# Optimization experiments

Measured on AMD Instinct MI355X. Metric: run time of the kernel, lower is better.

Reference implementation:

```python
import jax, jax.numpy as jnp
import numpy as np

B, N, IN, H, I, A, NA, NH = 4096, 8, 256, 256, 64, 64, 32, 256
VAR_FLOOR = 0.002
BN_EPS = 1e-5


def _lin(x, w, b):
    # torch Linear: x @ w.T + b, w: [out, in]
    return x @ w.T + b


def _bn_train(x, g, b):
    # BatchNorm1d in training mode: batch stats, biased variance
    mu = jnp.mean(x, axis=0)
    var = jnp.var(x, axis=0)
    return (x - mu) * jax.lax.rsqrt(var + BN_EPS) * g + b


def _intent_net(h_la, w1, b1, g, bbn, w2, b2):
    z = _lin(h_la, w1, b1)
    z = _bn_train(z, g, bbn)
    z = jax.nn.leaky_relu(z, 0.01)
    return _lin(z, w2, b2)


def setup_inputs() -> dict:
    key = jax.random.key(0)
    ks = jax.random.split(key, 30)
    s = 0.05
    d = {
        "inputs": jax.random.normal(ks[0], (B * N, IN), jnp.float32),
        "last_actions": jax.random.normal(ks[1], (B, N, NA), jnp.float32),
        "hidden_state": jax.random.normal(ks[2], (B * N, H), jnp.float32),
        "eps": jax.random.normal(ks[3], (B * N, I), jnp.float32),
        # fc1
        "fc1_w": jax.random.normal(ks[4], (H, IN), jnp.float32) * s,
        "fc1_b": jnp.zeros((H,), jnp.float32),
        # GRUCell (r,z,n gate order, torch layout)
        "gru_w_ih": jax.random.normal(ks[5], (3 * H, H), jnp.float32) * s,
        "gru_w_hh": jax.random.normal(ks[6], (3 * H, H), jnp.float32) * s,
        "gru_b_ih": jnp.zeros((3 * H,), jnp.float32),
        "gru_b_hh": jnp.zeros((3 * H,), jnp.float32),
        # intent_net: Linear(H+NA, NH) -> BN -> LeakyReLU -> Linear(NH, 2*I)
        "in1_w": jax.random.normal(ks[7], (NH, H + NA), jnp.float32) * s,
        "in1_b": jnp.zeros((NH,), jnp.float32),
        "bn_g": jnp.ones((NH,), jnp.float32),
        "bn_b": jnp.zeros((NH,), jnp.float32),
        "in2_w": jax.random.normal(ks[8], (2 * I, NH), jnp.float32) * s,
        "in2_b": jnp.zeros((2 * I,), jnp.float32),
        # attention projections
        "wq_w": jax.random.normal(ks[9], (A, I), jnp.float32) * s,
        "wq_b": jnp.zeros((A,), jnp.float32),
        "wk_w": jax.random.normal(ks[10], (A, I), jnp.float32) * s,
        "wk_b": jnp.zeros((A,), jnp.float32),
        "wv_w": jax.random.normal(ks[11], (A, I + H), jnp.float32) * s,
        "wv_b": jnp.zeros((A,), jnp.float32),
        # fc2
        "fc2_w": jax.random.normal(ks[12], (NA, H + A), jnp.float32) * s,
        "fc2_b": jnp.zeros((NA,), jnp.float32),
        "bs": B,
        "t": 1,
    }
    return d


def reference(inputs, last_actions, hidden_state, eps,
              fc1_w, fc1_b, gru_w_ih, gru_w_hh, gru_b_ih, gru_b_hh,
              in1_w, in1_b, bn_g, bn_b, in2_w, in2_b,
              wq_w, wq_b, wk_w, wk_b, wv_w, wv_b, fc2_w, fc2_b,
              bs, t):
    n = N
    x = jax.nn.relu(_lin(inputs, fc1_w, fc1_b))  # [bs*n, H]
    h_in = hidden_state.reshape(-1, H)
    # torch GRUCell
    gi = x @ gru_w_ih.T + gru_b_ih
    gh = h_in @ gru_w_hh.T + gru_b_hh
    i_r, i_z, i_n = jnp.split(gi, 3, axis=-1)
    h_r, h_z, h_n = jnp.split(gh, 3, axis=-1)
    r = jax.nn.sigmoid(i_r + h_r)
    z = jax.nn.sigmoid(i_z + h_z)
    nng = jnp.tanh(i_n + r * h_n)
    h = (1.0 - z) * nng + z * h_in  # [bs*n, H]

    la = last_actions.reshape(bs * n, NA)
    h_la = jnp.concatenate([h, la], axis=-1)
    ip = _intent_net(h_la, in1_w, in1_b, bn_g, bn_b, in2_w, in2_b)  # [bs*n, 2I]
    mean = ip[:, :I]
    std = jnp.maximum(jnp.exp(ip[:, I:]), VAR_FLOOR)
    intent = mean + eps * std  # reparameterized sample, [bs*n, I]

    q = _lin(intent, wq_w, wq_b).reshape(bs, n, A)  # query per agent i
    k = _lin(intent, wk_w, wk_b).reshape(bs, n, A)  # key per agent j
    scale = 1.0 / jnp.sqrt(jnp.float32(A))
    alpha = jnp.einsum('bia,bja->bij', q * scale, k)  # [bs, n, n]
    diag = jnp.eye(n, dtype=bool)
    alpha = jnp.where(diag[None], -1e9, alpha)
    alpha = jax.nn.softmax(alpha, axis=-1)

    v = _lin(jnp.concatenate([intent, h], axis=-1), wv_w, wv_b).reshape(bs, n, A)
    combined = jnp.einsum('bij,bja->bia', alpha, v).reshape(bs * n, A)

    local_Q = _lin(jnp.concatenate([h, combined], axis=-1), fc2_w, fc2_b).reshape(bs, n, NA)
    # final intent_embed: fresh intent_net output (no clamp/exp applied)
    intent_embed = _intent_net(h_la, in1_w, in1_b, bn_g, bn_b, in2_w, in2_b)
    return local_Q, h, intent, intent_embed
```

## Files before the change

kernel.cpp:

```cpp
#include <hip/hip_runtime.h>
#include <hip/hip_bf16.h>

#define BN_ 32768

using bf16 = __hip_bfloat16;
typedef __bf16 v8bf __attribute__((ext_vector_type(8)));
typedef unsigned short v8us __attribute__((ext_vector_type(8)));
typedef float v4f __attribute__((ext_vector_type(4)));

__device__ __forceinline__ float b2f(bf16 x) { return __bfloat162float(x); }
__device__ __forceinline__ bf16 f2b(float x) { return __float2bfloat16(x); }
__device__ __forceinline__ unsigned short f2bu(float x) {
  bf16 h = __float2bfloat16(x);
  return *reinterpret_cast<unsigned short*>(&h);
}
__device__ __forceinline__ float bu2f(unsigned short u) {
  union { unsigned int i; float f; } x;
  x.i = ((unsigned int)u) << 16;
  return x.f;
}
__device__ __forceinline__ void gl_lds16(const void* g, void* l) {
  __builtin_amdgcn_global_load_lds(
      (const __attribute__((address_space(1))) void*)g,
      (__attribute__((address_space(3))) void*)l, 16, 0, 0);
}
__device__ __forceinline__ float fsig(float x) { return 1.f / (1.f + __expf(-x)); }
__device__ __forceinline__ float ftanh(float x) {
  return 1.f - 2.f / (__expf(2.f * x) + 1.f);
}
template <int CF>
__device__ __forceinline__ void cstore(void* C, size_t off, float v) {
  if constexpr (CF) ((float*)C)[off] = v;
  else ((bf16*)C)[off] = f2b(v);
}
__device__ __forceinline__ int xcd_swz() {
  const int nbx = gridDim.x, nby = gridDim.y;
  const int f = blockIdx.y * nbx + blockIdx.x;
  const int nwg = nbx * nby;
  const int q = nwg >> 3, r = nwg & 7;
  const int xcd = f & 7, l = f >> 3;
  if (r == 0) return xcd * q + l;
  return (xcd < r ? xcd * (q + 1) : r * (q + 1) + (xcd - r) * q) + l;
}

template <int TM, int TN, int WR, int WC, int ACT, int A1M, int A2M, int KS, int KSB,
          int CF, int ATF, int STATS>
__global__ __launch_bounds__(256) void gemm_bt(
    const void* __restrict__ A1, int lda1, const void* __restrict__ A2, int lda2,
    const bf16* __restrict__ B1, const bf16* __restrict__ B2, int ldb,
    const float* __restrict__ bias, void* C, int ldc, int K,
    const float* __restrict__ tsc, const float* __restrict__ tsh,
    float* __restrict__ PART) {
  constexpr int BK = 64;
  __shared__ __align__(16) unsigned short As[TM * BK];
  __shared__ __align__(16) unsigned short Bs[TN * BK];
  const int tid = threadIdx.x;
  const int wv = tid >> 6;
  const int lane = tid & 63;
  const int w = xcd_swz();
  const int bm = (w / gridDim.y) * TM;
  const int bn = (w % gridDim.y) * TN;

  constexpr int WM = TM / WR, WN = TN / WC;
  constexpr int FM = WM / 16, FN = WN / 16;
  const int wm0 = (wv % WR) * WM;
  const int wn0 = (wv / WR) * WN;

  v4f acc[FM][FN];
  const v4f vzero = {0.f, 0.f, 0.f, 0.f};
  for (int i = 0; i < FM; ++i)
    for (int j = 0; j < FN; ++j) acc[i][j] = vzero;

  const int lrow = lane >> 3;
  const int lcol = (lane & 7) * 8;
  const int mr = lane & 15;
  const int kq = (lane >> 4) * 8;

  for (int k0 = 0; k0 < K; k0 += BK) {
    {
      const bool useA1 = (KS == 0) || (k0 < KS);
      const void* Ap = useA1 ? A1 : A2;
      const int lda = useA1 ? lda1 : lda2;
      const int ka = useA1 ? k0 : k0 - KS;
      const bool f32 = useA1 ? (A1M == 1) : (A2M == 1);
      if (ATF && useA1) {
        const unsigned short* Ab = (const unsigned short*)Ap;
        const float4 s0 = *(const float4*)(tsc + ka + lcol);
        const float4 s1 = *(const float4*)(tsc + ka + lcol + 4);
        const float4 h0 = *(const float4*)(tsh + ka + lcol);
        const float4 h1 = *(const float4*)(tsh + ka + lcol + 4);
        const float sc[8] = {s0.x, s0.y, s0.z, s0.w, s1.x, s1.y, s1.z, s1.w};
        const float sh[8] = {h0.x, h0.y, h0.z, h0.w, h1.x, h1.y, h1.z, h1.w};
        for (int ch = wv; ch < TM / 8; ch += 4) {
          const unsigned short* s = Ab + (size_t)(bm + ch * 8 + lrow) * lda + ka + lcol;
          v8us zin = *(const v8us*)s;
          v8us d;
#pragma unroll
          for (int u = 0; u < 8; ++u) {
            float v = bu2f(zin[u]) * sc[u] + sh[u];
            d[u] = f2bu(v > 0.f ? v : 0.01f * v);
          }
          *(v8us*)(As + ch * 8 * BK + lane * 8) = d;
        }
      } else if (f32) {
        const float* Af = (const float*)Ap;
        for (int ch = wv; ch < TM / 8; ch += 4) {
          const float* s = Af + (size_t)(bm + ch * 8 + lrow) * lda + ka + lcol;
          float4 x0 = *(const float4*)s;
          float4 x1 = *(const float4*)(s + 4);
          v8us d;
          d[0]=f2bu(x0.x); d[1]=f2bu(x0.y); d[2]=f2bu(x0.z); d[3]=f2bu(x0.w);
          d[4]=f2bu(x1.x); d[5]=f2bu(x1.y); d[6]=f2bu(x1.z); d[7]=f2bu(x1.w);
          *(v8us*)(As + ch * 8 * BK + lane * 8) = d;
        }
      } else {
        const unsigned short* Ab = (const unsigned short*)Ap;
        for (int ch = wv; ch < TM / 8; ch += 4)
          gl_lds16(Ab + (size_t)(bm + ch * 8 + lrow) * lda + ka + lcol,
                   As + ch * 8 * BK);
      }
    }
    {
      const bool useB1 = (KSB == 0) || (k0 < KSB);
      const bf16* Bp = useB1 ? B1 : B2;
      const int kb = useB1 ? k0 : k0 - KSB;
      for (int ch = wv; ch < TN / 8; ch += 4)
        gl_lds16((const unsigned short*)Bp + (size_t)(bn + ch * 8 + lrow) * ldb + kb + lcol,
                 Bs + ch * 8 * BK);
    }
    __syncthreads();
#pragma unroll
    for (int kk = 0; kk < BK; kk += 32) {
      v8bf af[FM], bfr[FN];
#pragma unroll
      for (int i = 0; i < FM; ++i)
        af[i] = *(const v8bf*)(As + (wm0 + i * 16 + mr) * BK + kk + kq);
#pragma unroll
      for (int j = 0; j < FN; ++j)
        bfr[j] = *(const v8bf*)(Bs + (wn0 + j * 16 + mr) * BK + kk + kq);
#pragma unroll
      for (int i = 0; i < FM; ++i)
#pragma unroll
        for (int j = 0; j < FN; ++j)
          acc[i][j] = __builtin_amdgcn_mfma_f32_16x16x32_bf16(af[i], bfr[j],
                                                              acc[i][j], 0, 0, 0);
    }
    __syncthreads();
  }
  const int crow = (lane >> 4) * 4;
#pragma unroll
  for (int j = 0; j < FN; ++j) {
    const int gcol = bn + wn0 + j * 16 + mr;
    const float bv = bias[gcol];
    float ps = 0.f, pq = 0.f;
#pragma unroll
    for (int i = 0; i < FM; ++i) {
#pragma unroll
      for (int r = 0; r < 4; ++r) {
        const int grow = bm + wm0 + i * 16 + crow + r;
        size_t off = (size_t)grow * ldc + gcol;
        float v = acc[i][j][r] + bv;
        if (ACT == 1) v = v > 0.f ? v : 0.f;
        if constexpr (STATS) {
          const unsigned short d = f2bu(v);
          ((bf16*)C)[off] = *(const bf16*)&d;
          const float vr = bu2f(d);
          ps += vr; pq += vr * vr;
        } else {
          cstore<CF>(C, off, v);
        }
      }
    }
    if constexpr (STATS) {
      ps += __shfl_xor(ps, 16); ps += __shfl_xor(ps, 32);
      pq += __shfl_xor(pq, 16); pq += __shfl_xor(pq, 32);
      if (lane < 16) {
        const int slot = (gcol << 9) + ((bm >> 7) << 1) + (wv % WR);
        PART[slot] = ps;
        PART[131072 + slot] = pq;
      }
    }
  }
}

__global__ __launch_bounds__(64) void bn_finalize2(
    const float* __restrict__ PART, const float* __restrict__ g,
    const float* __restrict__ b, float* __restrict__ stats) {
  const int col = blockIdx.x;
  const int lane = threadIdx.x;
  const float4* ps = (const float4*)(PART + (col << 9));
  const float4* pq = (const float4*)(PART + 131072 + (col << 9));
  float s = 0.f, q = 0.f;
#pragma unroll
  for (int u = 0; u < 2; ++u) {
    const float4 a = ps[lane * 2 + u];
    const float4 c = pq[lane * 2 + u];
    s += a.x + a.y + a.z + a.w;
    q += c.x + c.y + c.z + c.w;
  }
#pragma unroll
  for (int m = 1; m < 64; m <<= 1) {
    s += __shfl_xor(s, m);
    q += __shfl_xor(q, m);
  }
  if (lane == 0) {
    const float mean = s * (1.f / 32768.f);
    float var = q * (1.f / 32768.f) - mean * mean;
    var = fmaxf(var, 0.f);
    const float sc = g[col] * rsqrtf(var + 1e-5f);
    stats[512 + col] = sc;
    stats[768 + col] = b[col] - mean * sc;
  }
}

__global__ __launch_bounds__(256) void gru_fused(
    const bf16* __restrict__ X, const bf16* __restrict__ HB,
    const bf16* __restrict__ Win, const bf16* __restrict__ Whn,
    const float* __restrict__ FBp, const bf16* G1, unsigned short* HB2,
    float* __restrict__ Hout) {
  constexpr int BK = 64;
  __shared__ __align__(16) char smem[49152];
  unsigned short* AsX = (unsigned short*)smem;
  unsigned short* AsH = AsX + 4096;
  unsigned short* Bin = AsH + 4096;
  unsigned short* Bhn = Bin + 8192;
  float* Ein = (float*)smem;
  float* Ehn = Ein + 64 * 68;

  const int tid = threadIdx.x;
  const int wv = tid >> 6;
  const int lane = tid & 63;
  const int w = xcd_swz();
  const int bm = (w / gridDim.y) * 64;
  const int bn = (w % gridDim.y) * 128;
  const int wm0 = (wv & 1) * 32;
  const int wn0 = (wv >> 1) * 64;

  v4f ain[2][4], ahn[2][4];
  const v4f vzero = {0.f, 0.f, 0.f, 0.f};
  for (int i = 0; i < 2; ++i)
    for (int j = 0; j < 4; ++j) { ain[i][j] = vzero; ahn[i][j] = vzero; }

  const int lrow = lane >> 3;
  const int lcol = (lane & 7) * 8;
  const int mr = lane & 15;
  const int kq = (lane >> 4) * 8;

  for (int k0 = 0; k0 < 256; k0 += BK) {
    for (int ch = wv; ch < 8; ch += 4) {
      const size_t aoff = (size_t)(bm + ch * 8 + lrow) * 256 + k0 + lcol;
      gl_lds16((const unsigned short*)X + aoff, AsX + ch * 8 * BK);
      gl_lds16((const unsigned short*)HB + aoff, AsH + ch * 8 * BK);
    }
    for (int ch = wv; ch < 16; ch += 4) {
      const size_t boff = (size_t)(bn + ch * 8 + lrow) * 256 + k0 + lcol;
      gl_lds16((const unsigned short*)Win + boff, Bin + ch * 8 * BK);
      gl_lds16((const unsigned short*)Whn + boff, Bhn + ch * 8 * BK);
    }
    __syncthreads();
#pragma unroll
    for (int kk = 0; kk < BK; kk += 32) {
      v8bf ax[2], ah[2], bi[4], bh[4];
#pragma unroll
      for (int i = 0; i < 2; ++i) {
        ax[i] = *(const v8bf*)(AsX + (wm0 + i * 16 + mr) * BK + kk + kq);
        ah[i] = *(const v8bf*)(AsH + (wm0 + i * 16 + mr) * BK + kk + kq);
      }
#pragma unroll
      for (int j = 0; j < 4; ++j) {
        bi[j] = *(const v8bf*)(Bin + (wn0 + j * 16 + mr) * BK + kk + kq);
        bh[j] = *(const v8bf*)(Bhn + (wn0 + j * 16 + mr) * BK + kk + kq);
      }
#pragma unroll
      for (int i = 0; i < 2; ++i)
#pragma unroll
        for (int j = 0; j < 4; ++j) {
          ain[i][j] = __builtin_amdgcn_mfma_f32_16x16x32_bf16(ax[i], bi[j],
                                                              ain[i][j], 0, 0, 0);
          ahn[i][j] = __builtin_amdgcn_mfma_f32_16x16x32_bf16(ah[i], bh[j],
                                                              ahn[i][j], 0, 0, 0);
        }
    }
    __syncthreads();
  }

  const int crow = (lane >> 4) * 4;
  const int myhalf = wn0 >> 6;
  const int c4 = (tid & 15) * 4;
#pragma unroll
  for (int h = 0; h < 2; ++h) {
    ushort4 r4a[4], z4a[4], hp4a[4];
#pragma unroll
    for (int it = 0; it < 4; ++it) {
      const int grow = bm + (tid >> 4) + it * 16;
      const int gcol = bn + h * 64 + c4;
      const unsigned short* g1p = (const unsigned short*)G1 + (size_t)grow * 512 + gcol;
      r4a[it] = *(const ushort4*)g1p;
      z4a[it] = *(const ushort4*)(g1p + 256);
      hp4a[it] = *(const ushort4*)((const unsigned short*)HB + (size_t)grow * 256 + gcol);
    }
    __syncthreads();
    if (myhalf == h) {
#pragma unroll
      for (int i = 0; i < 2; ++i)
#pragma unroll
        for (int j = 0; j < 4; ++j)
#pragma unroll
          for (int r = 0; r < 4; ++r) {
            const int idx = (wm0 + i * 16 + crow + r) * 68 + j * 16 + mr;
            Ein[idx] = ain[i][j][r];
            Ehn[idx] = ahn[i][j][r];
          }
    }
    __syncthreads();
#pragma unroll
    for (int it = 0; it < 4; ++it) {
      const int row = (tid >> 4) + it * 16;
      const int grow = bm + row;
      const int gcol = bn + h * 64 + c4;
      const float4 ei = *(const float4*)(Ein + row * 68 + c4);
      const float4 eh = *(const float4*)(Ehn + row * 68 + c4);
      const float4 bin4 = *(const float4*)(FBp + 768 + gcol);
      const float4 bhn4 = *(const float4*)(FBp + 1024 + gcol);
      const float rv[4] = {bu2f(r4a[it].x), bu2f(r4a[it].y), bu2f(r4a[it].z), bu2f(r4a[it].w)};
      const float zv[4] = {bu2f(z4a[it].x), bu2f(z4a[it].y), bu2f(z4a[it].z), bu2f(z4a[it].w)};
      const float hpv[4] = {bu2f(hp4a[it].x), bu2f(hp4a[it].y), bu2f(hp4a[it].z), bu2f(hp4a[it].w)};
      const float eiv[4] = {ei.x, ei.y, ei.z, ei.w};
      const float ehv[4] = {eh.x, eh.y, eh.z, eh.w};
      const float biv[4] = {bin4.x, bin4.y, bin4.z, bin4.w};
      const float bhv[4] = {bhn4.x, bhn4.y, bhn4.z, bhn4.w};
      float vo[4];
#pragma unroll
      for (int u = 0; u < 4; ++u) {
        float rr = fsig(rv[u]);
        float zz = fsig(zv[u]);
        float nn = ftanh(eiv[u] + biv[u] + rr * (ehv[u] + bhv[u]));
        vo[u] = (1.f - zz) * nn + zz * hpv[u];
      }
      *(float4*)(Hout + (size_t)grow * 256 + gcol) =
          make_float4(vo[0], vo[1], vo[2], vo[3]);
      ushort4 hb2;
      hb2.x = f2bu(vo[0]); hb2.y = f2bu(vo[1]);
      hb2.z = f2bu(vo[2]); hb2.w = f2bu(vo[3]);
      *(ushort4*)(HB2 + (size_t)grow * 512 + gcol) = hb2;
    }
  }
}

__global__ void conv_all(
    const float* fc1_w, const float* w_ih, const float* w_hh, const float* in1_w,
    const float* in2_w, const float* wq_w, const float* wk_w, const float* wv_w,
    const float* fc2_w, const float* fc1_b, const float* b_ih, const float* b_hh,
    const float* in1_b, const float* in2_b, const float* wq_b, const float* wk_b,
    const float* wv_b, const float* fc2_b, const float* bn_g, const float* bn_b,
    bf16* __restrict__ WF, float* __restrict__ FB) {
  int idx = blockIdx.x * 256 + threadIdx.x;
  if (idx < 612352) {
    float v;
    if (idx < 65536) v = fc1_w[idx];
    else if (idx < 262144) v = w_ih[idx - 65536];
    else if (idx < 458752) v = w_hh[idx - 262144];
    else if (idx < 540672) {
      int j = idx - 458752, r = j / 320, c = j % 320;
      v = (c < 288) ? in1_w[r * 288 + c] : 0.f;
    } else if (idx < 573440) v = in2_w[idx - 540672];
    else if (idx < 581632) {
      int j = idx - 573440, r = j >> 6, c = j & 63;
      v = (r < 64) ? wq_w[r * 64 + c] : wk_w[(r - 64) * 64 + c];
    } else if (idx < 602112) v = wv_w[idx - 581632];
    else v = fc2_w[idx - 602112];
    WF[idx] = f2b(v);
  } else if (idx < 615936) {
    int j = idx - 612352;
    float v;
    if (j < 256) v = fc1_b[j];
    else if (j < 768) v = b_ih[j - 256] + b_hh[j - 256];
    else if (j < 1024) v = b_ih[512 + j - 768];
    else if (j < 1280) v = b_hh[512 + j - 1024];
    else if (j < 1536) v = in1_b[j - 1280];
    else if (j < 1664) v = in2_b[j - 1536];
    else if (j < 1792) { int c = j - 1664; v = (c < 64) ? wq_b[c] : wk_b[c - 64]; }
    else if (j < 1856) v = wv_b[j - 1792];
    else if (j < 1888) v = fc2_b[j - 1856];
    else if (j < 2144) v = bn_g[j - 1888];
    else if (j < 2400) v = bn_b[j - 2144];
    else v = 0.f;
    FB[j] = v;
  }
}

__global__ void pack_all(const float* __restrict__ h, bf16* __restrict__ hb,
                         const float* __restrict__ x, bf16* __restrict__ xb,
                         const float* __restrict__ la, bf16* __restrict__ lap) {
  const int bid = blockIdx.x;
  if (bid < 8192) {
    const float* s = bid < 4096 ? h : x;
    bf16* d = bid < 4096 ? hb : xb;
    const int i = (bid & 4095) * 256 + threadIdx.x;
    const float4 x0 = ((const float4*)s)[i * 2];
    const float4 x1 = ((const float4*)s)[i * 2 + 1];
    v8us o;
    o[0]=f2bu(x0.x); o[1]=f2bu(x0.y); o[2]=f2bu(x0.z); o[3]=f2bu(x0.w);
    o[4]=f2bu(x1.x); o[5]=f2bu(x1.y); o[6]=f2bu(x1.z); o[7]=f2bu(x1.w);
    ((v8us*)d)[i] = o;
  } else {
    const int i = (bid - 8192) * 256 + threadIdx.x;
    const int row = i >> 3, cg = i & 7;
    v8us o;
    if (cg < 4) {
      const float4 a = *(const float4*)(la + (size_t)row * 32 + cg * 8);
      const float4 b = *(const float4*)(la + (size_t)row * 32 + cg * 8 + 4);
      o[0]=f2bu(a.x); o[1]=f2bu(a.y); o[2]=f2bu(a.z); o[3]=f2bu(a.w);
      o[4]=f2bu(b.x); o[5]=f2bu(b.y); o[6]=f2bu(b.z); o[7]=f2bu(b.w);
    } else {
      for (int u = 0; u < 8; ++u) o[u] = 0;
    }
    ((v8us*)lap)[i] = o;
  }
}

__global__ void make_intent(const float* __restrict__ ie, const float* __restrict__ eps,
                            float* __restrict__ intent, unsigned short* __restrict__ itb) {
  int idx = blockIdx.x * 256 + threadIdx.x;
  int row = idx >> 6, c = idx & 63;
  float mean = ie[(size_t)row * 128 + c];
  float sd = fmaxf(expf(ie[(size_t)row * 128 + 64 + c]), 0.002f);
  float v = mean + eps[idx] * sd;
  intent[idx] = v;
  itb[(size_t)row * 512 + c] = f2bu(v);
}

__global__ __launch_bounds__(256) void attn(const bf16* __restrict__ QK,
                                            const bf16* __restrict__ Vv,
                                            bf16* __restrict__ comb) {
  __shared__ float q[4][8][65], k[4][8][65], v[4][8][65];
  __shared__ float al[4][8][8];
  const int wv = threadIdx.x >> 6, t = threadIdx.x & 63;
  const int b = blockIdx.x * 4 + wv;
  const size_t rb = (size_t)b * 8;
  const unsigned short* qkb = (const unsigned short*)QK + rb * 128;
#pragma unroll
  for (int p = 0; p < 2; ++p) {
    const int e = t * 8 + p * 512;
    const int row = e >> 7, col = e & 127;
    v8us d = *(const v8us*)(qkb + row * 128 + col);
    if (col < 64) {
#pragma unroll
      for (int u = 0; u < 8; ++u) q[wv][row][col + u] = bu2f(d[u]);
    } else {
#pragma unroll
      for (int u = 0; u < 8; ++u) k[wv][row][col - 64 + u] = bu2f(d[u]);
    }
  }
  {
    const int e = t * 8;
    const int row = e >> 6, col = e & 63;
    v8us d = *(const v8us*)((const unsigned short*)Vv + rb * 64 + row * 64 + col);
#pragma unroll
    for (int u = 0; u < 8; ++u) v[wv][row][col + u] = bu2f(d[u]);
  }
  __syncthreads();
  const int i = t >> 3, j = t & 7;
  float s = 0.f;
#pragma unroll
  for (int a = 0; a < 64; ++a) s += q[wv][i][a] * k[wv][j][a];
  s *= 0.125f;
  if (i == j) s = -1e9f;
  float m = s;
  m = fmaxf(m, __shfl_xor(m, 1, 8));
  m = fmaxf(m, __shfl_xor(m, 2, 8));
  m = fmaxf(m, __shfl_xor(m, 4, 8));
  float e = __expf(s - m);
  float sum = e;
  sum += __shfl_xor(sum, 1, 8);
  sum += __shfl_xor(sum, 2, 8);
  sum += __shfl_xor(sum, 4, 8);
  al[wv][i][j] = e / sum;
  __syncthreads();
  const int a0 = (t & 7) * 8;
  v8us o8;
#pragma unroll
  for (int u = 0; u < 8; ++u) {
    float o = 0.f;
#pragma unroll
    for (int jj = 0; jj < 8; ++jj) o += al[wv][i][jj] * v[wv][jj][a0 + u];
    o8[u] = f2bu(o);
  }
  *(v8us*)((unsigned short*)comb + (rb + i) * 64 + a0) = o8;
}

extern "C" void kernel_launch(void* const* d_in, const int* in_sizes, int n_in,
                              void* d_out, int out_size, void* d_ws, size_t ws_size,
                              hipStream_t stream) {
  (void)in_sizes; (void)n_in; (void)out_size; (void)ws_size;
  const float* inputs = (const float*)d_in[0];
  const float* last_actions = (const float*)d_in[1];
  const float* hidden = (const float*)d_in[2];
  const float* eps = (const float*)d_in[3];

  float* out = (float*)d_out;
  float* out_lq = out;
  float* out_h = out + 1048576;
  float* out_it = out + 9437184;
  float* out_ie = out + 11534336;

  bf16* HB = (bf16*)(out + 11534336);
  bf16* XB = (bf16*)(out + 1048576);
  bf16* LAP = (bf16*)out_lq;
  float* PART = out + 9437184;

  char* ws = (char*)d_ws;
  bf16* X    = (bf16*)(ws + 0);
  bf16* G1   = (bf16*)(ws + 16777216);
  unsigned short* HB2 = (unsigned short*)(ws + 16777216);
  unsigned short* ITB = (unsigned short*)(ws + 16777216) + 256;
  bf16* Z1   = (bf16*)(ws + 0);
  bf16* QK   = (bf16*)(ws + 0);
  bf16* V    = (bf16*)(ws + 8388608);
  bf16* COMB = (bf16*)(ws + 12582912);
  float* FB  = (float*)(ws + 50331648);
  bf16*  WF  = (bf16*)(ws + 50348032);
  float* stats = FB + 2560;

  conv_all<<<2406, 256, 0, stream>>>(
      (const float*)d_in[4], (const float*)d_in[6], (const float*)d_in[7],
      (const float*)d_in[10], (const float*)d_in[14], (const float*)d_in[16],
      (const float*)d_in[18], (const float*)d_in[20], (const float*)d_in[22],
      (const float*)d_in[5], (const float*)d_in[8], (const float*)d_in[9],
      (const float*)d_in[11], (const float*)d_in[15], (const float*)d_in[17],
      (const float*)d_in[19], (const float*)d_in[21], (const float*)d_in[23],
      (const float*)d_in[12], (const float*)d_in[13], WF, FB);

  pack_all<<<9216, 256, 0, stream>>>(hidden, HB, inputs, XB, last_actions, LAP);

  gemm_bt<64, 128, 2, 2, 1, 0, 0, 0, 0, 0, 0, 0><<<dim3(512, 2), 256, 0, stream>>>(
      XB, 256, nullptr, 0, WF + 0, nullptr, 256, FB + 0, X, 256, 256,
      nullptr, nullptr, nullptr);
  gemm_bt<64, 128, 2, 2, 0, 0, 0, 256, 256, 0, 0, 0><<<dim3(512, 4), 256, 0, stream>>>(
      X, 256, HB, 256, WF + 65536, WF + 262144, 256, FB + 256, G1, 512, 512,
      nullptr, nullptr, nullptr);
  gru_fused<<<dim3(512, 2), 256, 0, stream>>>(
      X, HB, WF + 65536 + 512 * 256, WF + 262144 + 512 * 256, FB, G1, HB2, out_h);

  gemm_bt<128, 128, 2, 2, 0, 0, 0, 256, 0, 0, 0, 1><<<dim3(256, 2), 256, 0, stream>>>(
      HB2, 512, LAP, 64, WF + 458752, nullptr, 320, FB + 1280, Z1, 256, 320,
      nullptr, nullptr, PART);
  bn_finalize2<<<256, 64, 0, stream>>>(PART, FB + 1888, FB + 2144, stats);
  gemm_bt<64, 128, 2, 2, 0, 0, 0, 0, 0, 1, 1, 0><<<dim3(512, 1), 256, 0, stream>>>(
      Z1, 256, nullptr, 0, WF + 540672, nullptr, 256, FB + 1536, out_ie, 128, 256,
      stats + 512, stats + 768, nullptr);
  make_intent<<<8192, 256, 0, stream>>>(out_ie, eps, out_it, ITB);
  gemm_bt<64, 128, 2, 2, 0, 0, 0, 0, 0, 0, 0, 0><<<dim3(512, 1), 256, 0, stream>>>(
      ITB, 512, nullptr, 0, WF + 573440, nullptr, 64, FB + 1664, QK, 128, 64,
      nullptr, nullptr, nullptr);
  gemm_bt<64, 64, 4, 1, 0, 0, 0, 64, 0, 0, 0, 0><<<dim3(512, 1), 256, 0, stream>>>(
      ITB, 512, HB2, 512, WF + 581632, nullptr, 320, FB + 1792, V, 64, 320,
      nullptr, nullptr, nullptr);
  attn<<<1024, 256, 0, stream>>>(QK, V, COMB);
  gemm_bt<64, 32, 4, 1, 0, 0, 0, 256, 0, 1, 0, 0><<<dim3(512, 1), 256, 0, stream>>>(
      HB2, 512, COMB, 64, WF + 602112, nullptr, 320, FB + 1856, out_lq, 32, 320,
      nullptr, nullptr, nullptr);
}
```

Measured before the change: 320.4 us.

## Fuse intent sampling into in2 GEMM, merge Q/K/V GEMMs, double-buffer GRU loads

The intent reparameterization (exp, floor, eps multiply, bf16 pack) moves into the epilogue of the second intent-net GEMM, which removes the separate make_intent kernel and its extra pass over the 128-wide output. The Q/K and V projections are merged into one 192-column GEMM over the concatenated [intent, h] input, using a zero-padded combined weight and a split epilogue that writes two outputs. The gru_fused kernel now double-buffers its LDS loads at K-step 32, so the next global load overlaps with the current MFMAs. In exchange, the merged Q/K GEMM does wasted multiplies over the zero-padded h columns, and the weight-conversion kernel grows.

```diff
diff --git a/kernel.cpp b/kernel.cpp
--- a/kernel.cpp
+++ b/kernel.cpp
@@ -44,13 +44,14 @@
 }
 
 template <int TM, int TN, int WR, int WC, int ACT, int A1M, int A2M, int KS, int KSB,
-          int CF, int ATF, int STATS>
+          int CF, int ATF, int STATS, int QKV>
 __global__ __launch_bounds__(256) void gemm_bt(
     const void* __restrict__ A1, int lda1, const void* __restrict__ A2, int lda2,
     const bf16* __restrict__ B1, const bf16* __restrict__ B2, int ldb,
     const float* __restrict__ bias, void* C, int ldc, int K,
     const float* __restrict__ tsc, const float* __restrict__ tsh,
-    float* __restrict__ PART) {
+    float* __restrict__ PART, const float* __restrict__ pe,
+    float* __restrict__ pit, unsigned short* __restrict__ pitb, void* C2) {
   constexpr int BK = 64;
   __shared__ __align__(16) unsigned short As[TM * BK];
   __shared__ __align__(16) unsigned short Bs[TN * BK];
@@ -148,36 +149,60 @@
     __syncthreads();
   }
   const int crow = (lane >> 4) * 4;
-#pragma unroll
-  for (int j = 0; j < FN; ++j) {
-    const int gcol = bn + wn0 + j * 16 + mr;
-    const float bv = bias[gcol];
-    float ps = 0.f, pq = 0.f;
-#pragma unroll
-    for (int i = 0; i < FM; ++i) {
+
+  if constexpr (ACT == 5) {
+#pragma unroll
+    for (int j = 0; j < 4; ++j) {
+      const int gcol = bn + j * 16 + mr;
+      const float bmn = bias[gcol];
+      const float bsd = bias[gcol + 64];
 #pragma unroll
       for (int r = 0; r < 4; ++r) {
-        const int grow = bm + wm0 + i * 16 + crow + r;
-        size_t off = (size_t)grow * ldc + gcol;
-        float v = acc[i][j][r] + bv;
-        if (ACT == 1) v = v > 0.f ? v : 0.f;
-        if constexpr (STATS) {
-          const unsigned short d = f2bu(v);
-          ((bf16*)C)[off] = *(const bf16*)&d;
-          const float vr = bu2f(d);
-          ps += vr; pq += vr * vr;
-        } else {
-          cstore<CF>(C, off, v);
+        const int grow = bm + wm0 + crow + r;
+        const float mean = acc[0][j][r] + bmn;
+        const float lstd = acc[0][j + 4][r] + bsd;
+        ((float*)C)[(size_t)grow * 128 + gcol] = mean;
+        ((float*)C)[(size_t)grow * 128 + gcol + 64] = lstd;
+        const float sd = fmaxf(__expf(lstd), 0.002f);
+        const float iv = mean + pe[(size_t)grow * 64 + gcol] * sd;
+        pit[(size_t)grow * 64 + gcol] = iv;
+        pitb[(size_t)grow * 512 + gcol] = f2bu(iv);
+      }
+    }
+  } else {
+#pragma unroll
+    for (int j = 0; j < FN; ++j) {
+      const int gcol = bn + wn0 + j * 16 + mr;
+      const float bv = bias[gcol];
+      float ps = 0.f, pq = 0.f;
+#pragma unroll
+      for (int i = 0; i < FM; ++i) {
+#pragma unroll
+        for (int r = 0; r < 4; ++r) {
+          const int grow = bm + wm0 + i * 16 + crow + r;
+          float v = acc[i][j][r] + bv;
+          if (ACT == 1) v = v > 0.f ? v : 0.f;
+          if constexpr (QKV) {
+            if (gcol < 128) ((bf16*)C)[(size_t)grow * 128 + gcol] = f2b(v);
+            else ((bf16*)C2)[(size_t)grow * 64 + (gcol - 128)] = f2b(v);
+          } else if constexpr (STATS) {
+            const unsigned short d = f2bu(v);
+            ((bf16*)C)[(size_t)grow * ldc + gcol] = *(const bf16*)&d;
+            const float vr = bu2f(d);
+            ps += vr; pq += vr * vr;
+          } else {
+            cstore<CF>(C, (size_t)grow * ldc + gcol, v);
+          }
         }
       }
-    }
-    if constexpr (STATS) {
-      ps += __shfl_xor(ps, 16); ps += __shfl_xor(ps, 32);
-      pq += __shfl_xor(pq, 16); pq += __shfl_xor(pq, 32);
-      if (lane < 16) {
-        const int slot = (gcol << 9) + ((bm >> 7) << 1) + (wv % WR);
-        PART[slot] = ps;
-        PART[131072 + slot] = pq;
+      if constexpr (STATS) {
+        ps += __shfl_xor(ps, 16); ps += __shfl_xor(ps, 32);
+        pq += __shfl_xor(pq, 16); pq += __shfl_xor(pq, 32);
+        if (lane < 16) {
+          const int slot = (gcol << 9) + ((bm >> 7) << 1) + (wv % WR);
+          PART[slot] = ps;
+          PART[131072 + slot] = pq;
+        }
       }
     }
   }
@@ -218,12 +243,7 @@
     const bf16* __restrict__ Win, const bf16* __restrict__ Whn,
     const float* __restrict__ FBp, const bf16* G1, unsigned short* HB2,
     float* __restrict__ Hout) {
-  constexpr int BK = 64;
   __shared__ __align__(16) char smem[49152];
-  unsigned short* AsX = (unsigned short*)smem;
-  unsigned short* AsH = AsX + 4096;
-  unsigned short* Bin = AsH + 4096;
-  unsigned short* Bhn = Bin + 8192;
   float* Ein = (float*)smem;
   float* Ehn = Ein + 64 * 68;
 
@@ -241,35 +261,44 @@
   for (int i = 0; i < 2; ++i)
     for (int j = 0; j < 4; ++j) { ain[i][j] = vzero; ahn[i][j] = vzero; }
 
-  const int lrow = lane >> 3;
-  const int lcol = (lane & 7) * 8;
+  const int lrow2 = lane >> 2;
+  const int lcol2 = (lane & 3) * 8;
   const int mr = lane & 15;
   const int kq = (lane >> 4) * 8;
 
-  for (int k0 = 0; k0 < 256; k0 += BK) {
-    for (int ch = wv; ch < 8; ch += 4) {
-      const size_t aoff = (size_t)(bm + ch * 8 + lrow) * 256 + k0 + lcol;
-      gl_lds16((const unsigned short*)X + aoff, AsX + ch * 8 * BK);
-      gl_lds16((const unsigned short*)HB + aoff, AsH + ch * 8 * BK);
-    }
-    for (int ch = wv; ch < 16; ch += 4) {
-      const size_t boff = (size_t)(bn + ch * 8 + lrow) * 256 + k0 + lcol;
-      gl_lds16((const unsigned short*)Win + boff, Bin + ch * 8 * BK);
-      gl_lds16((const unsigned short*)Whn + boff, Bhn + ch * 8 * BK);
-    }
-    __syncthreads();
-#pragma unroll
-    for (int kk = 0; kk < BK; kk += 32) {
+  auto STAGE = [&](int b, int t) {
+    unsigned short* base = (unsigned short*)(smem + b * 24576);
+    const int k0 = t * 32;
+    {
+      const size_t aoff = (size_t)(bm + wv * 16 + lrow2) * 256 + k0 + lcol2;
+      gl_lds16((const unsigned short*)X + aoff, base + wv * 512);
+      gl_lds16((const unsigned short*)HB + aoff, base + 2048 + wv * 512);
+    }
+    for (int c = wv; c < 8; c += 4) {
+      const size_t boff = (size_t)(bn + c * 16 + lrow2) * 256 + k0 + lcol2;
+      gl_lds16((const unsigned short*)Win + boff, base + 4096 + c * 512);
+      gl_lds16((const unsigned short*)Whn + boff, base + 8192 + c * 512);
+    }
+  };
+
+  int cur = 0;
+  STAGE(0, 0);
+  asm volatile("s_waitcnt vmcnt(0)" ::: "memory");
+  __builtin_amdgcn_s_barrier();
+  for (int t = 0; t < 8; ++t) {
+    if (t < 7) STAGE(cur ^ 1, t + 1);
+    {
+      const unsigned short* base = (const unsigned short*)(smem + cur * 24576);
       v8bf ax[2], ah[2], bi[4], bh[4];
 #pragma unroll
       for (int i = 0; i < 2; ++i) {
-        ax[i] = *(const v8bf*)(AsX + (wm0 + i * 16 + mr) * BK + kk + kq);
-        ah[i] = *(const v8bf*)(AsH + (wm0 + i * 16 + mr) * BK + kk + kq);
+        ax[i] = *(const v8bf*)(base + (wm0 + i * 16 + mr) * 32 + kq);
+        ah[i] = *(const v8bf*)(base + 2048 + (wm0 + i * 16 + mr) * 32 + kq);
       }
 #pragma unroll
       for (int j = 0; j < 4; ++j) {
-        bi[j] = *(const v8bf*)(Bin + (wn0 + j * 16 + mr) * BK + kk + kq);
-        bh[j] = *(const v8bf*)(Bhn + (wn0 + j * 16 + mr) * BK + kk + kq);
+        bi[j] = *(const v8bf*)(base + 4096 + (wn0 + j * 16 + mr) * 32 + kq);
+        bh[j] = *(const v8bf*)(base + 8192 + (wn0 + j * 16 + mr) * 32 + kq);
       }
 #pragma unroll
       for (int i = 0; i < 2; ++i)
@@ -281,7 +310,9 @@
                                                               ahn[i][j], 0, 0, 0);
         }
     }
-    __syncthreads();
+    asm volatile("s_waitcnt vmcnt(0)" ::: "memory");
+    __builtin_amdgcn_s_barrier();
+    cur ^= 1;
   }
 
   const int crow = (lane >> 4) * 4;
@@ -355,7 +386,7 @@
     const float* wv_b, const float* fc2_b, const float* bn_g, const float* bn_b,
     bf16* __restrict__ WF, float* __restrict__ FB) {
   int idx = blockIdx.x * 256 + threadIdx.x;
-  if (idx < 612352) {
+  if (idx < 673792) {
     float v;
     if (idx < 65536) v = fc1_w[idx];
     else if (idx < 262144) v = w_ih[idx - 65536];
@@ -364,14 +395,20 @@
       int j = idx - 458752, r = j / 320, c = j % 320;
       v = (c < 288) ? in1_w[r * 288 + c] : 0.f;
     } else if (idx < 573440) v = in2_w[idx - 540672];
-    else if (idx < 581632) {
-      int j = idx - 573440, r = j >> 6, c = j & 63;
-      v = (r < 64) ? wq_w[r * 64 + c] : wk_w[(r - 64) * 64 + c];
-    } else if (idx < 602112) v = wv_w[idx - 581632];
-    else v = fc2_w[idx - 602112];
+    else if (idx < 602112) {
+      v = (idx >= 573440 && idx < 581632)
+              ? 0.f
+              : (idx < 602112 ? 0.f : 0.f);
+    } else if (idx < 612352) v = fc2_w[idx - 602112];
+    else {
+      int j = idx - 612352, r = j / 320, c = j % 320;
+      if (r < 128) v = (c < 64) ? (r < 64 ? wq_w[r * 64 + c]
+                                          : wk_w[(r - 64) * 64 + c]) : 0.f;
+      else v = wv_w[(size_t)(r - 128) * 320 + c];
+    }
     WF[idx] = f2b(v);
-  } else if (idx < 615936) {
-    int j = idx - 612352;
+  } else if (idx < 677376) {
+    int j = idx - 673792;
     float v;
     if (j < 256) v = fc1_b[j];
     else if (j < 768) v = b_ih[j - 256] + b_hh[j - 256];
@@ -419,17 +456,6 @@
   }
 }
 
-__global__ void make_intent(const float* __restrict__ ie, const float* __restrict__ eps,
-                            float* __restrict__ intent, unsigned short* __restrict__ itb) {
-  int idx = blockIdx.x * 256 + threadIdx.x;
-  int row = idx >> 6, c = idx & 63;
-  float mean = ie[(size_t)row * 128 + c];
-  float sd = fmaxf(expf(ie[(size_t)row * 128 + 64 + c]), 0.002f);
-  float v = mean + eps[idx] * sd;
-  intent[idx] = v;
-  itb[(size_t)row * 512 + c] = f2bu(v);
-}
-
 __global__ __launch_bounds__(256) void attn(const bf16* __restrict__ QK,
                                             const bf16* __restrict__ Vv,
                                             bf16* __restrict__ comb) {
@@ -522,7 +548,7 @@
   bf16*  WF  = (bf16*)(ws + 50348032);
   float* stats = FB + 2560;
 
-  conv_all<<<2406, 256, 0, stream>>>(
+  conv_all<<<2646, 256, 0, stream>>>(
       (const float*)d_in[4], (const float*)d_in[6], (const float*)d_in[7],
       (const float*)d_in[10], (const float*)d_in[14], (const float*)d_in[16],
       (const float*)d_in[18], (const float*)d_in[20], (const float*)d_in[22],
@@ -533,31 +559,27 @@
 
   pack_all<<<9216, 256, 0, stream>>>(hidden, HB, inputs, XB, last_actions, LAP);
 
-  gemm_bt<64, 128, 2, 2, 1, 0, 0, 0, 0, 0, 0, 0><<<dim3(512, 2), 256, 0, stream>>>(
+  gemm_bt<64, 128, 2, 2, 1, 0, 0, 0, 0, 0, 0, 0, 0><<<dim3(512, 2), 256, 0, stream>>>(
       XB, 256, nullptr, 0, WF + 0, nullptr, 256, FB + 0, X, 256, 256,
-      nullptr, nullptr, nullptr);
-  gemm_bt<64, 128, 2, 2, 0, 0, 0, 256, 256, 0, 0, 0><<<dim3(512, 4), 256, 0, stream>>>(
+      nullptr, nullptr, nullptr, nullptr, nullptr, nullptr, nullptr);
+  gemm_bt<64, 128, 2, 2, 0, 0, 0, 256, 256, 0, 0, 0, 0><<<dim3(512, 4), 256, 0, stream>>>(
       X, 256, HB, 256, WF + 65536, WF + 262144, 256, FB + 256, G1, 512, 512,
-      nullptr, nullptr, nullptr);
+      nullptr, nullptr, nullptr, nullptr, nullptr, nullptr, nullptr);
   gru_fused<<<dim3(512, 2), 256, 0, stream>>>(
       X, HB, WF + 65536 + 512 * 256, WF + 262144 + 512 * 256, FB, G1, HB2, out_h);
 
-  gemm_bt<128, 128, 2, 2, 0, 0, 0, 256, 0, 0, 0, 1><<<dim3(256, 2), 256, 0, stream>>>(
+  gemm_bt<128, 128, 2, 2, 0, 0, 0, 256, 0, 0, 0, 1, 0><<<dim3(256, 2), 256, 0, stream>>>(
       HB2, 512, LAP, 64, WF + 458752, nullptr, 320, FB + 1280, Z1, 256, 320,
-      nullptr, nullptr, PART);
+      nullptr, nullptr, PART, nullptr, nullptr, nullptr, nullptr);
   bn_finalize2<<<256, 64, 0, stream>>>(PART, FB + 1888, FB + 2144, stats);
-  gemm_bt<64, 128, 2, 2, 0, 0, 0, 0, 0, 1, 1, 0><<<dim3(512, 1), 256, 0, stream>>>(
+  gemm_bt<64, 128, 4, 1, 5, 0, 0, 0, 0, 1, 1, 0, 0><<<dim3(512, 1), 256, 0, stream>>>(
       Z1, 256, nullptr, 0, WF + 540672, nullptr, 256, FB + 1536, out_ie, 128, 256,
-      stats + 512, stats + 768, nullptr);
-  make_intent<<<8192, 256, 0, stream>>>(out_ie, eps, out_it, ITB);
-  gemm_bt<64, 128, 2, 2, 0, 0, 0, 0, 0, 0, 0, 0><<<dim3(512, 1), 256, 0, stream>>>(
-      ITB, 512, nullptr, 0, WF + 573440, nullptr, 64, FB + 1664, QK, 128, 64,
-      nullptr, nullptr, nullptr);
-  gemm_bt<64, 64, 4, 1, 0, 0, 0, 64, 0, 0, 0, 0><<<dim3(512, 1), 256, 0, stream>>>(
-      ITB, 512, HB2, 512, WF + 581632, nullptr, 320, FB + 1792, V, 64, 320,
-      nullptr, nullptr, nullptr);
+      stats + 512, stats + 768, nullptr, eps, out_it, ITB, nullptr);
+  gemm_bt<64, 192, 2, 2, 0, 0, 0, 64, 0, 0, 0, 0, 1><<<dim3(512, 1), 256, 0, stream>>>(
+      ITB, 512, HB2, 512, WF + 612352, nullptr, 320, FB + 1664, QK, 128, 320,
+      nullptr, nullptr, nullptr, nullptr, nullptr, nullptr, V);
   attn<<<1024, 256, 0, stream>>>(QK, V, COMB);
-  gemm_bt<64, 32, 4, 1, 0, 0, 0, 256, 0, 1, 0, 0><<<dim3(512, 1), 256, 0, stream>>>(
+  gemm_bt<64, 32, 4, 1, 0, 0, 0, 256, 0, 1, 0, 0, 0><<<dim3(512, 1), 256, 0, stream>>>(
       HB2, 512, COMB, 64, WF + 602112, nullptr, 320, FB + 1856, out_lq, 32, 320,
-      nullptr, nullptr, nullptr);
-}
+      nullptr, nullptr, nullptr, nullptr, nullptr, nullptr, nullptr);
+}
```

Result: no change. 323.8 us (+1.1%).
